# Performance work log

Hardware: AMD Instinct MI355X
Metric: run time of the kernel (lower is better)

Reference implementation:

```python
import jax, jax.numpy as jnp
import numpy as np

N_NODES = 100000
N_EDGES = 3200000


def _gcn_conv(x, src, dst, W, b, n):
    # symmetric GCN normalization with self-loops (PyG GCNConv default)
    deg = jax.ops.segment_sum(jnp.ones_like(dst, dtype=x.dtype), dst, num_segments=n)
    dinv = jnp.where(deg > 0, jax.lax.rsqrt(jnp.maximum(deg, 1e-12)), 0.0)
    norm = dinv[src] * dinv[dst]                       # [E+N]
    h = x @ W                                          # [n, out]
    msg = h[src] * norm[:, None]                       # gather + scale
    out = jax.ops.segment_sum(msg, dst, num_segments=n)  # scatter-add
    return out + b


def setup_inputs() -> dict:
    key = jax.random.key(0)
    k1, k2, k3, k4 = jax.random.split(key, 4)
    feat = jax.random.normal(k1, (N_NODES, 1), dtype=jnp.float32)
    edge_ix = jax.random.randint(k2, (2, N_EDGES), 0, N_NODES, dtype=jnp.int64)
    W1 = jax.random.normal(k3, (1, 32), dtype=jnp.float32) * (1.0 / 1.0)
    b1 = jnp.zeros((32,), dtype=jnp.float32)
    W2 = jax.random.normal(k4, (32, 64), dtype=jnp.float32) * (1.0 / np.sqrt(32.0))
    b2 = jnp.zeros((64,), dtype=jnp.float32)
    return {"feat": feat, "edge_ix": edge_ix, "W1": W1, "b1": b1, "W2": W2, "b2": b2}


def reference(feat, edge_ix, W1, b1, W2, b2):
    n = feat.shape[0]
    # add self loops once; reuse for both layers
    loops = jnp.arange(n, dtype=edge_ix.dtype)
    src = jnp.concatenate([edge_ix[0], loops])
    dst = jnp.concatenate([edge_ix[1], loops])
    x = jax.nn.relu(_gcn_conv(feat, src, dst, W1, b1, n))
    x = jax.nn.relu(_gcn_conv(x, src, dst, W2, b2, n))
    return x
```

## Files before the change

### kernel.cpp

```cpp
#include <hip/hip_runtime.h>


#define TPB 256
#define TPBW 1024
#define NSBMAX 1024
#define SBSZ 256
#define LBITS 8
#define SPLIT 4

__global__ void k_detect(const int* __restrict__ e32, int E, int* __restrict__ flag,
                         int* __restrict__ gHist, int NSB) {
    __shared__ int ok;
    if (threadIdx.x == 0) ok = 1;
    __syncthreads();
    for (int i = threadIdx.x; i < NSB; i += TPB) gHist[i] = 0;
    int stride = E / 2048; if (stride < 1) stride = 1;
    bool bad = false;
#pragma unroll
    for (int i = 0; i < 8; ++i) {
        long k = (long)(threadIdx.x * 8 + i) * stride + 1;
        if (k < E && e32[2 * k + 1] != 0) bad = true;
    }
    if (bad) atomicAnd(&ok, 0);
    __syncthreads();
    if (threadIdx.x == 0) *flag = ok;
}

__global__ void k_uv(const float* __restrict__ W1, const float* __restrict__ b1,
                     const float* __restrict__ W2, float* __restrict__ upm,
                     int* __restrict__ bzero) {
    __shared__ float sw[32], sb[32];
    int k = threadIdx.x;
    if (k < 32) { sw[k] = W1[k]; sb[k] = b1[k]; }
    __syncthreads();
    float up = 0.f, um = 0.f;
#pragma unroll
    for (int c = 0; c < 32; ++c) {
        float w = sw[c];
        float w2 = W2[c * 64 + k];
        up = fmaf(fmaxf(w, 0.f), w2, up);
        um = fmaf(fmaxf(-w, 0.f), w2, um);
    }
    upm[k] = up;
    upm[64 + k] = um;
    if (k == 0) {
        int z = 1;
        for (int c = 0; c < 32; ++c) if (sb[c] != 0.f) z = 0;
        *bzero = z;
    }
}

__global__ void k_hist(const int* __restrict__ e32, const int* __restrict__ flag,
                       int E, int NSB, int* __restrict__ gHist) {
    __shared__ int sh[NSBMAX];
    for (int i = threadIdx.x; i < NSB; i += TPBW) sh[i] = 0;
    __syncthreads();
    int f = *flag;
    long stride = (long)gridDim.x * TPBW;
    for (long e = (long)blockIdx.x * TPBW + threadIdx.x; e < E; e += stride) {
        int d = e32[((long)E + e) << f];
        atomicAdd(&sh[d >> LBITS], 1);
    }
    __syncthreads();
    for (int i = threadIdx.x; i < NSB; i += TPBW)
        if (sh[i]) atomicAdd(&gHist[i], sh[i]);
}

__global__ void k_scan(const int* __restrict__ gHist, int NSB, int E,
                       int* __restrict__ base, int* __restrict__ cursor) {
    __shared__ int s[TPB];
    int K = (NSB + TPB - 1) / TPB;
    int t = threadIdx.x;
    int i0 = t * K;
    int tot = 0;
    for (int k = 0; k < K; ++k) { int i = i0 + k; if (i < NSB) tot += gHist[i]; }
    s[t] = tot;
    __syncthreads();
    for (int off = 1; off < TPB; off <<= 1) {
        int v = s[t];
        int u = (t >= off) ? s[t - off] : 0;
        __syncthreads();
        s[t] = v + u;
        __syncthreads();
    }
    int run = s[t] - tot;
    for (int k = 0; k < K; ++k) {
        int i = i0 + k;
        if (i < NSB) { int h = gHist[i]; base[i] = run; cursor[i] = run; run += h; }
    }
    if (t == 0) base[NSB] = E;
}

__global__ void k_part(const int* __restrict__ e32, const int* __restrict__ flag,
                       int E, int NSB, int* __restrict__ cursor,
                       unsigned int* __restrict__ P, int chunk) {
    __shared__ int sh[NSBMAX];
    int c0 = blockIdx.x * chunk;
    int c1 = c0 + chunk; if (c1 > E) c1 = E;
    for (int i = threadIdx.x; i < NSB; i += TPBW) sh[i] = 0;
    __syncthreads();
    int f = *flag;
    for (int e = c0 + threadIdx.x; e < c1; e += TPBW) {
        int d = e32[((long)E + e) << f];
        atomicAdd(&sh[d >> LBITS], 1);
    }
    __syncthreads();
    for (int i = threadIdx.x; i < NSB; i += TPBW) {
        int c = sh[i];
        sh[i] = c ? atomicAdd(&cursor[i], c) : 0;
    }
    __syncthreads();
    int sshift = 32 - LBITS;
    for (int e = c0 + threadIdx.x; e < c1; e += TPBW) {
        long ee = (long)e << f;
        int s = e32[ee];
        int d = e32[(((long)E) << f) + ee];
        int b = d >> LBITS;
        int pos = atomicAdd(&sh[b], 1);
        P[pos] = (unsigned)s | ((unsigned)(d & (SBSZ - 1)) << sshift);
    }
}

__global__ void k_degS(const unsigned int* __restrict__ P, const int* __restrict__ base,
                       int n, int* __restrict__ cntP) {
    __shared__ int cnt[SBSZ];
    int bb = blockIdx.x / SPLIT, pp = blockIdx.x % SPLIT;
    int t = threadIdx.x;
    cnt[t] = 0;
    __syncthreads();
    int p0 = base[bb], len = base[bb + 1] - p0;
    int s0 = p0 + (int)((long)len * pp / SPLIT);
    int s1 = p0 + (int)((long)len * (pp + 1) / SPLIT);
    int sshift = 32 - LBITS;
    for (int p = s0 + t; p < s1; p += TPB)
        atomicAdd(&cnt[P[p] >> sshift], 1);
    __syncthreads();
    int v = (bb << LBITS) + t;
    if (v < n) cntP[pp * n + v] = cnt[t];
}

__global__ void k_prep1(const int* __restrict__ cntP, const float* __restrict__ feat,
                        int n, float* __restrict__ dinv, float* __restrict__ g) {
    int v = blockIdx.x * TPB + threadIdx.x;
    if (v >= n) return;
    int c = 0;
#pragma unroll
    for (int pp = 0; pp < SPLIT; ++pp) c += cntP[pp * n + v];
    float di = rsqrtf((float)(c + 1));
    dinv[v] = di;
    g[v] = di * feat[v];
}

__global__ void k_aggAS(const unsigned int* __restrict__ P, const int* __restrict__ base,
                        int n, const float* __restrict__ g, float* __restrict__ AP) {
    __shared__ float A[SBSZ];
    int bb = blockIdx.x / SPLIT, pp = blockIdx.x % SPLIT;
    int t = threadIdx.x;
    A[t] = 0.f;
    __syncthreads();
    int p0 = base[bb], len = base[bb + 1] - p0;
    int s0 = p0 + (int)((long)len * pp / SPLIT);
    int s1 = p0 + (int)((long)len * (pp + 1) / SPLIT);
    int sshift = 32 - LBITS;
    unsigned smask = (1u << sshift) - 1;
    for (int p = s0 + t; p < s1; p += TPB) {
        unsigned e = P[p];
        atomicAdd(&A[e >> sshift], g[e & smask]);
    }
    __syncthreads();
    int v = (bb << LBITS) + t;
    if (v < n) AP[pp * n + v] = A[t];
}

__global__ void k_prep2(const float* __restrict__ AP, const float* __restrict__ g,
                        const float* __restrict__ dinv, int n, const int* __restrict__ bzero,
                        float* __restrict__ qs, float2* __restrict__ pd,
                        float* __restrict__ Yagg) {
    int v = blockIdx.x * TPB + threadIdx.x;
    if (v >= n) return;
    float A = g[v];
#pragma unroll
    for (int pp = 0; pp < SPLIT; ++pp) A += AP[pp * n + v];
    float di = dinv[v];
    float px = di * A;
    qs[v] = di * px;
    if (!*bzero) {
        pd[v] = make_float2(px, di);
        float4* Y = (float4*)(Yagg + (size_t)v * 32);
#pragma unroll
        for (int i = 0; i < 8; ++i) Y[i] = make_float4(0.f, 0.f, 0.f, 0.f);
    }
}

__global__ void k_aggTS(const unsigned int* __restrict__ P, const int* __restrict__ base,
                        int n, const float* __restrict__ qs, float2* __restrict__ SP2) {
    __shared__ float Sp[SBSZ], Sm[SBSZ];
    int bb = blockIdx.x / SPLIT, pp = blockIdx.x % SPLIT;
    int t = threadIdx.x;
    Sp[t] = 0.f; Sm[t] = 0.f;
    __syncthreads();
    int p0 = base[bb], len = base[bb + 1] - p0;
    int s0 = p0 + (int)((long)len * pp / SPLIT);
    int s1 = p0 + (int)((long)len * (pp + 1) / SPLIT);
    int sshift = 32 - LBITS;
    unsigned smask = (1u << sshift) - 1;
    for (int p = s0 + t; p < s1; p += TPB) {
        unsigned e = P[p];
        float q = qs[e & smask];
        int l = e >> sshift;
        float* addr = (q >= 0.f) ? &Sp[l] : &Sm[l];
        atomicAdd(addr, fabsf(q));
    }
    __syncthreads();
    int v = (bb << LBITS) + t;
    if (v < n) SP2[pp * n + v] = make_float2(Sp[t], Sm[t]);
}

__global__ void k_out(const float* __restrict__ qs, const float* __restrict__ dinv,
                      const float2* __restrict__ SP2, const float* __restrict__ upm,
                      const float* __restrict__ b2, const int* __restrict__ bzero,
                      int n, float* __restrict__ out) {
    if (!*bzero) return;
    __shared__ float su[192];
    if (threadIdx.x < 192) su[threadIdx.x] = (threadIdx.x < 128) ? upm[threadIdx.x] : b2[threadIdx.x - 128];
    __syncthreads();
    int o = blockIdx.x * TPB + threadIdx.x;
    if (o >= n * 64) return;
    int v = o >> 6, k = o & 63;
    float qv = qs[v];
    float Sp = fmaxf(qv, 0.f), Sm = fmaxf(-qv, 0.f);
#pragma unroll
    for (int pp = 0; pp < SPLIT; ++pp) { float2 s = SP2[pp * n + v]; Sp += s.x; Sm += s.y; }
    float r = fmaf(dinv[v], fmaf(Sp, su[k], Sm * su[64 + k]), su[128 + k]);
    out[o] = fmaxf(r, 0.f);
}

__global__ void k_aggY(const int* __restrict__ e32, const int* __restrict__ flag,
                       int E, const int* __restrict__ bzero,
                       const float2* __restrict__ pd,
                       const float* __restrict__ W1, const float* __restrict__ b1,
                       float* __restrict__ Yagg) {
    if (*bzero) return;
    __shared__ float sw[32], sb[32];
    if (threadIdx.x < 32) { sw[threadIdx.x] = W1[threadIdx.x]; sb[threadIdx.x] = b1[threadIdx.x]; }
    __syncthreads();
    int sh = *flag;
    long stride = (long)gridDim.x * TPB;
    for (long e = (long)blockIdx.x * TPB + threadIdx.x; e < E; e += stride) {
        int s = e32[e << sh];
        int d = e32[((long)E + e) << sh];
        float2 p = pd[s];
#pragma unroll
        for (int c = 0; c < 32; ++c) {
            float y = p.y * fmaxf(fmaf(sw[c], p.x, sb[c] * p.y), 0.f);
            atomicAdd(&Yagg[(size_t)d * 32 + c], y);
        }
    }
}

__global__ void k_final_gen(const float2* __restrict__ pd, const float* __restrict__ Yagg,
                            const float* __restrict__ W1, const float* __restrict__ b1,
                            const float* __restrict__ W2, const float* __restrict__ b2,
                            const int* __restrict__ bzero, int n, float* __restrict__ out) {
    if (*bzero) return;
    __shared__ float sW[32 * 64];
    __shared__ float sb2[64];
    __shared__ float sagg[8][33];
    int t = threadIdx.x;
    for (int i = t; i < 32 * 64; i += TPB) sW[i] = W2[i];
    if (t < 64) sb2[t] = b2[t];
    int vl = t >> 5, c = t & 31;
    int nblk = (n + 7) / 8;
    for (int blk = blockIdx.x; blk < nblk; blk += gridDim.x) {
        int v = blk * 8 + vl;
        float a = 0.f;
        if (v < n) {
            float2 p = pd[v];
            float dv = p.y;
            float yv = fmaxf(fmaf(W1[c], p.x, b1[c] * p.y), 0.f);
            a = dv * (dv * yv + Yagg[(size_t)v * 32 + c]);
        }
        __syncthreads();
        sagg[vl][c] = a;
        __syncthreads();
        if (v < n) {
            float o0 = sb2[c], o1 = sb2[c + 32];
#pragma unroll
            for (int j = 0; j < 32; ++j) {
                float x = sagg[vl][j];
                o0 += x * sW[j * 64 + c];
                o1 += x * sW[j * 64 + 32 + c];
            }
            out[(size_t)v * 64 + c]      = fmaxf(o0, 0.f);
            out[(size_t)v * 64 + 32 + c] = fmaxf(o1, 0.f);
        }
    }
}

static inline size_t align256(size_t x) { return (x + 255) & ~(size_t)255; }

extern "C" void kernel_launch(void* const* d_in, const int* in_sizes, int n_in,
                              void* d_out, int out_size, void* d_ws, size_t ws_size,
                              hipStream_t stream) {
    const float* feat = (const float*)d_in[0];
    const int*   e32  = (const int*)d_in[1];
    const float* W1   = (const float*)d_in[2];
    const float* b1   = (const float*)d_in[3];
    const float* W2   = (const float*)d_in[4];
    const float* b2   = (const float*)d_in[5];
    float* out = (float*)d_out;

    int n = in_sizes[0];
    int E = in_sizes[1] / 2;

    int NSB = (n + SBSZ - 1) >> LBITS;

    char* w = (char*)d_ws;
    size_t off = 0;
    auto alloc = [&](size_t bytes) -> char* { char* p = w + off; off = align256(off + bytes); return p; };
    unsigned int* P = (unsigned int*)alloc((size_t)E * 4);
    int*    gHist = (int*)alloc((size_t)NSB * 4);
    int*    base  = (int*)alloc((size_t)(NSB + 1) * 4);
    int*    cursor= (int*)alloc((size_t)NSB * 4);
    int*    cntP  = (int*)alloc((size_t)SPLIT * n * 4);
    float*  AP    = (float*)alloc((size_t)SPLIT * n * 4);
    float2* SP2   = (float2*)alloc((size_t)SPLIT * n * 8);
    float*  dinv  = (float*)alloc((size_t)n * 4);
    float*  g     = (float*)alloc((size_t)n * 4);
    float*  qs    = (float*)alloc((size_t)n * 4);
    float2* pd    = (float2*)alloc((size_t)n * 8);
    float*  upm   = (float*)alloc(128 * 4);
    int*    flag  = (int*)alloc(4);
    int*    bzero = (int*)alloc(4);
    float*  Yagg  = (float*)alloc((size_t)n * 32 * 4);

    int chunk = (E + 255) / 256;
    int gC = (E + chunk - 1) / chunk;
    int gN = (n + TPB - 1) / TPB;
    int gS = NSB * SPLIT;
    int gO = (n * 64 + TPB - 1) / TPB;

    hipLaunchKernelGGL(k_detect,    dim3(1),    dim3(TPB),  0, stream, e32, E, flag, gHist, NSB);
    hipLaunchKernelGGL(k_uv,        dim3(1),    dim3(64),   0, stream, W1, b1, W2, upm, bzero);
    hipLaunchKernelGGL(k_hist,      dim3(256),  dim3(TPBW), 0, stream, e32, flag, E, NSB, gHist);
    hipLaunchKernelGGL(k_scan,      dim3(1),    dim3(TPB),  0, stream, gHist, NSB, E, base, cursor);
    hipLaunchKernelGGL(k_part,      dim3(gC),   dim3(TPBW), 0, stream, e32, flag, E, NSB, cursor, P, chunk);
    hipLaunchKernelGGL(k_degS,      dim3(gS),   dim3(TPB),  0, stream, P, base, n, cntP);
    hipLaunchKernelGGL(k_prep1,     dim3(gN),   dim3(TPB),  0, stream, cntP, feat, n, dinv, g);
    hipLaunchKernelGGL(k_aggAS,     dim3(gS),   dim3(TPB),  0, stream, P, base, n, g, AP);
    hipLaunchKernelGGL(k_prep2,     dim3(gN),   dim3(TPB),  0, stream, AP, g, dinv, n, bzero, qs, pd, Yagg);
    hipLaunchKernelGGL(k_aggTS,     dim3(gS),   dim3(TPB),  0, stream, P, base, n, qs, SP2);
    hipLaunchKernelGGL(k_out,       dim3(gO),   dim3(TPB),  0, stream, qs, dinv, SP2, upm, b2, bzero, n, out);
    hipLaunchKernelGGL(k_aggY,      dim3(512),  dim3(TPB),  0, stream, e32, flag, E, bzero, pd, W1, b1, Yagg);
    hipLaunchKernelGGL(k_final_gen, dim3(1024), dim3(TPB),  0, stream, pd, Yagg, W1, b1, W2, b2, bzero, n, out);
}
```

Measured before the change: 130.7 us.

## Replace atomic-cursor partition with per-chunk histograms and column scan

The bucket partition of edges by destination super-block now keeps a per-chunk histogram matrix, scans it per column in a new kernel, and gives each chunk exact write offsets. This drops the second per-chunk counting pass and the global atomic cursor claims inside the partition kernel. The detect and weight-precompute kernels are merged into one launch. In exchange it adds a column-scan launch and extra histogram/offset buffers of size chunks × buckets.

```diff
diff --git a/kernel.cpp b/kernel.cpp
--- a/kernel.cpp
+++ b/kernel.cpp
@@ -7,95 +7,52 @@
 #define SBSZ 256
 #define LBITS 8
 #define SPLIT 4
-
-__global__ void k_detect(const int* __restrict__ e32, int E, int* __restrict__ flag,
-                         int* __restrict__ gHist, int NSB) {
+#define NCHUNK 256
+
+__global__ void k_init(const int* __restrict__ e32, int E, int* __restrict__ flag,
+                       const float* __restrict__ W1, const float* __restrict__ b1,
+                       const float* __restrict__ W2, float* __restrict__ upm,
+                       int* __restrict__ bzero) {
     __shared__ int ok;
-    if (threadIdx.x == 0) ok = 1;
-    __syncthreads();
-    for (int i = threadIdx.x; i < NSB; i += TPB) gHist[i] = 0;
+    __shared__ float sw[32], sb[32];
+    int t = threadIdx.x;
+    if (t == 0) ok = 1;
+    if (t < 32) { sw[t] = W1[t]; sb[t] = b1[t]; }
+    __syncthreads();
     int stride = E / 2048; if (stride < 1) stride = 1;
     bool bad = false;
 #pragma unroll
     for (int i = 0; i < 8; ++i) {
-        long k = (long)(threadIdx.x * 8 + i) * stride + 1;
+        long k = (long)(t * 8 + i) * stride + 1;
         if (k < E && e32[2 * k + 1] != 0) bad = true;
     }
     if (bad) atomicAnd(&ok, 0);
-    __syncthreads();
-    if (threadIdx.x == 0) *flag = ok;
-}
-
-__global__ void k_uv(const float* __restrict__ W1, const float* __restrict__ b1,
-                     const float* __restrict__ W2, float* __restrict__ upm,
-                     int* __restrict__ bzero) {
-    __shared__ float sw[32], sb[32];
-    int k = threadIdx.x;
-    if (k < 32) { sw[k] = W1[k]; sb[k] = b1[k]; }
-    __syncthreads();
-    float up = 0.f, um = 0.f;
-#pragma unroll
-    for (int c = 0; c < 32; ++c) {
-        float w = sw[c];
-        float w2 = W2[c * 64 + k];
-        up = fmaf(fmaxf(w, 0.f), w2, up);
-        um = fmaf(fmaxf(-w, 0.f), w2, um);
-    }
-    upm[k] = up;
-    upm[64 + k] = um;
-    if (k == 0) {
+    if (t < 64) {
+        float up = 0.f, um = 0.f;
+#pragma unroll
+        for (int c = 0; c < 32; ++c) {
+            float w = sw[c];
+            float w2 = W2[c * 64 + t];
+            up = fmaf(fmaxf(w, 0.f), w2, up);
+            um = fmaf(fmaxf(-w, 0.f), w2, um);
+        }
+        upm[t] = up;
+        upm[64 + t] = um;
+    }
+    __syncthreads();
+    if (t == 0) {
+        *flag = ok;
         int z = 1;
         for (int c = 0; c < 32; ++c) if (sb[c] != 0.f) z = 0;
         *bzero = z;
     }
 }
 
-__global__ void k_hist(const int* __restrict__ e32, const int* __restrict__ flag,
-                       int E, int NSB, int* __restrict__ gHist) {
+__global__ void k_hist2(const int* __restrict__ e32, const int* __restrict__ flag,
+                        int E, int NSB, int chunk, int* __restrict__ H) {
     __shared__ int sh[NSBMAX];
-    for (int i = threadIdx.x; i < NSB; i += TPBW) sh[i] = 0;
-    __syncthreads();
-    int f = *flag;
-    long stride = (long)gridDim.x * TPBW;
-    for (long e = (long)blockIdx.x * TPBW + threadIdx.x; e < E; e += stride) {
-        int d = e32[((long)E + e) << f];
-        atomicAdd(&sh[d >> LBITS], 1);
-    }
-    __syncthreads();
-    for (int i = threadIdx.x; i < NSB; i += TPBW)
-        if (sh[i]) atomicAdd(&gHist[i], sh[i]);
-}
-
-__global__ void k_scan(const int* __restrict__ gHist, int NSB, int E,
-                       int* __restrict__ base, int* __restrict__ cursor) {
-    __shared__ int s[TPB];
-    int K = (NSB + TPB - 1) / TPB;
-    int t = threadIdx.x;
-    int i0 = t * K;
-    int tot = 0;
-    for (int k = 0; k < K; ++k) { int i = i0 + k; if (i < NSB) tot += gHist[i]; }
-    s[t] = tot;
-    __syncthreads();
-    for (int off = 1; off < TPB; off <<= 1) {
-        int v = s[t];
-        int u = (t >= off) ? s[t - off] : 0;
-        __syncthreads();
-        s[t] = v + u;
-        __syncthreads();
-    }
-    int run = s[t] - tot;
-    for (int k = 0; k < K; ++k) {
-        int i = i0 + k;
-        if (i < NSB) { int h = gHist[i]; base[i] = run; cursor[i] = run; run += h; }
-    }
-    if (t == 0) base[NSB] = E;
-}
-
-__global__ void k_part(const int* __restrict__ e32, const int* __restrict__ flag,
-                       int E, int NSB, int* __restrict__ cursor,
-                       unsigned int* __restrict__ P, int chunk) {
-    __shared__ int sh[NSBMAX];
-    int c0 = blockIdx.x * chunk;
+    int c = blockIdx.x;
+    int c0 = c * chunk;
     int c1 = c0 + chunk; if (c1 > E) c1 = E;
     for (int i = threadIdx.x; i < NSB; i += TPBW) sh[i] = 0;
     __syncthreads();
@@ -105,11 +62,64 @@
         atomicAdd(&sh[d >> LBITS], 1);
     }
     __syncthreads();
-    for (int i = threadIdx.x; i < NSB; i += TPBW) {
-        int c = sh[i];
-        sh[i] = c ? atomicAdd(&cursor[i], c) : 0;
-    }
-    __syncthreads();
+    for (int i = threadIdx.x; i < NSB; i += TPBW) H[(size_t)c * NSB + i] = sh[i];
+}
+
+__global__ void k_colscan(const int* __restrict__ H, int NSB,
+                          int* __restrict__ P2, int* __restrict__ colsum) {
+    __shared__ int s[NCHUNK];
+    int b = blockIdx.x, t = threadIdx.x;
+    int v = H[(size_t)t * NSB + b];
+    s[t] = v;
+    __syncthreads();
+    for (int off = 1; off < NCHUNK; off <<= 1) {
+        int x = s[t];
+        int u = (t >= off) ? s[t - off] : 0;
+        __syncthreads();
+        s[t] = x + u;
+        __syncthreads();
+    }
+    P2[(size_t)t * NSB + b] = s[t] - v;
+    if (t == NCHUNK - 1) colsum[b] = s[t];
+}
+
+__global__ void k_scan(const int* __restrict__ colsum, int NSB, int E,
+                       int* __restrict__ base) {
+    __shared__ int s[TPB];
+    int K = (NSB + TPB - 1) / TPB;
+    int t = threadIdx.x;
+    int i0 = t * K;
+    int tot = 0;
+    for (int k = 0; k < K; ++k) { int i = i0 + k; if (i < NSB) tot += colsum[i]; }
+    s[t] = tot;
+    __syncthreads();
+    for (int off = 1; off < TPB; off <<= 1) {
+        int v = s[t];
+        int u = (t >= off) ? s[t - off] : 0;
+        __syncthreads();
+        s[t] = v + u;
+        __syncthreads();
+    }
+    int run = s[t] - tot;
+    for (int k = 0; k < K; ++k) {
+        int i = i0 + k;
+        if (i < NSB) { base[i] = run; run += colsum[i]; }
+    }
+    if (t == 0) base[NSB] = E;
+}
+
+__global__ void k_part2(const int* __restrict__ e32, const int* __restrict__ flag,
+                        int E, int NSB, const int* __restrict__ base,
+                        const int* __restrict__ P2, unsigned int* __restrict__ P,
+                        int chunk) {
+    __shared__ int sh[NSBMAX];
+    int c = blockIdx.x;
+    int c0 = c * chunk;
+    int c1 = c0 + chunk; if (c1 > E) c1 = E;
+    for (int i = threadIdx.x; i < NSB; i += TPBW)
+        sh[i] = base[i] + P2[(size_t)c * NSB + i];
+    __syncthreads();
+    int f = *flag;
     int sshift = 32 - LBITS;
     for (int e = c0 + threadIdx.x; e < c1; e += TPBW) {
         long ee = (long)e << f;
@@ -319,9 +329,10 @@
     size_t off = 0;
     auto alloc = [&](size_t bytes) -> char* { char* p = w + off; off = align256(off + bytes); return p; };
     unsigned int* P = (unsigned int*)alloc((size_t)E * 4);
-    int*    gHist = (int*)alloc((size_t)NSB * 4);
+    int*    H     = (int*)alloc((size_t)NCHUNK * NSB * 4);
+    int*    P2    = (int*)alloc((size_t)NCHUNK * NSB * 4);
+    int*    colsum= (int*)alloc((size_t)NSB * 4);
     int*    base  = (int*)alloc((size_t)(NSB + 1) * 4);
-    int*    cursor= (int*)alloc((size_t)NSB * 4);
     int*    cntP  = (int*)alloc((size_t)SPLIT * n * 4);
     float*  AP    = (float*)alloc((size_t)SPLIT * n * 4);
     float2* SP2   = (float2*)alloc((size_t)SPLIT * n * 8);
@@ -334,23 +345,22 @@
     int*    bzero = (int*)alloc(4);
     float*  Yagg  = (float*)alloc((size_t)n * 32 * 4);
 
-    int chunk = (E + 255) / 256;
-    int gC = (E + chunk - 1) / chunk;
+    int chunk = (E + NCHUNK - 1) / NCHUNK;
     int gN = (n + TPB - 1) / TPB;
     int gS = NSB * SPLIT;
     int gO = (n * 64 + TPB - 1) / TPB;
 
-    hipLaunchKernelGGL(k_detect,    dim3(1),    dim3(TPB),  0, stream, e32, E, flag, gHist, NSB);
-    hipLaunchKernelGGL(k_uv,        dim3(1),    dim3(64),   0, stream, W1, b1, W2, upm, bzero);
-    hipLaunchKernelGGL(k_hist,      dim3(256),  dim3(TPBW), 0, stream, e32, flag, E, NSB, gHist);
-    hipLaunchKernelGGL(k_scan,      dim3(1),    dim3(TPB),  0, stream, gHist, NSB, E, base, cursor);
-    hipLaunchKernelGGL(k_part,      dim3(gC),   dim3(TPBW), 0, stream, e32, flag, E, NSB, cursor, P, chunk);
-    hipLaunchKernelGGL(k_degS,      dim3(gS),   dim3(TPB),  0, stream, P, base, n, cntP);
-    hipLaunchKernelGGL(k_prep1,     dim3(gN),   dim3(TPB),  0, stream, cntP, feat, n, dinv, g);
-    hipLaunchKernelGGL(k_aggAS,     dim3(gS),   dim3(TPB),  0, stream, P, base, n, g, AP);
-    hipLaunchKernelGGL(k_prep2,     dim3(gN),   dim3(TPB),  0, stream, AP, g, dinv, n, bzero, qs, pd, Yagg);
-    hipLaunchKernelGGL(k_aggTS,     dim3(gS),   dim3(TPB),  0, stream, P, base, n, qs, SP2);
-    hipLaunchKernelGGL(k_out,       dim3(gO),   dim3(TPB),  0, stream, qs, dinv, SP2, upm, b2, bzero, n, out);
-    hipLaunchKernelGGL(k_aggY,      dim3(512),  dim3(TPB),  0, stream, e32, flag, E, bzero, pd, W1, b1, Yagg);
-    hipLaunchKernelGGL(k_final_gen, dim3(1024), dim3(TPB),  0, stream, pd, Yagg, W1, b1, W2, b2, bzero, n, out);
-}
+    hipLaunchKernelGGL(k_init,      dim3(1),      dim3(TPB),  0, stream, e32, E, flag, W1, b1, W2, upm, bzero);
+    hipLaunchKernelGGL(k_hist2,     dim3(NCHUNK), dim3(TPBW), 0, stream, e32, flag, E, NSB, chunk, H);
+    hipLaunchKernelGGL(k_colscan,   dim3(NSB),    dim3(NCHUNK), 0, stream, H, NSB, P2, colsum);
+    hipLaunchKernelGGL(k_scan,      dim3(1),      dim3(TPB),  0, stream, colsum, NSB, E, base);
+    hipLaunchKernelGGL(k_part2,     dim3(NCHUNK), dim3(TPBW), 0, stream, e32, flag, E, NSB, base, P2, P, chunk);
+    hipLaunchKernelGGL(k_degS,      dim3(gS),     dim3(TPB),  0, stream, P, base, n, cntP);
+    hipLaunchKernelGGL(k_prep1,     dim3(gN),     dim3(TPB),  0, stream, cntP, feat, n, dinv, g);
+    hipLaunchKernelGGL(k_aggAS,     dim3(gS),     dim3(TPB),  0, stream, P, base, n, g, AP);
+    hipLaunchKernelGGL(k_prep2,     dim3(gN),     dim3(TPB),  0, stream, AP, g, dinv, n, bzero, qs, pd, Yagg);
+    hipLaunchKernelGGL(k_aggTS,     dim3(gS),     dim3(TPB),  0, stream, P, base, n, qs, SP2);
+    hipLaunchKernelGGL(k_out,       dim3(gO),     dim3(TPB),  0, stream, qs, dinv, SP2, upm, b2, bzero, n, out);
+    hipLaunchKernelGGL(k_aggY,      dim3(512),    dim3(TPB),  0, stream, e32, flag, E, bzero, pd, W1, b1, Yagg);
+    hipLaunchKernelGGL(k_final_gen, dim3(1024),   dim3(TPB),  0, stream, pd, Yagg, W1, b1, W2, b2, bzero, n, out);
+}
```

New measurement: 122.4 us. 6.4% less time.
